# Performance work log

Hardware: AMD Instinct MI355X
Metric: run time of the kernel (lower is better)

Reference implementation:

```python
import jax, jax.numpy as jnp
import numpy as np

B, N, H, KRATE = 128, 400, 128, 0.2
EPS = 1e-9


def setup_inputs() -> dict:
    key = jax.random.key(0)
    ks = jax.random.split(key, 16)
    # correlation-like input: symmetric, values in (-1,1), unit diagonal
    x = jax.random.normal(ks[0], (B, N, N), dtype=jnp.float32)
    x = jnp.tanh(0.3 * x)
    x = 0.5 * (x + x.transpose(0, 2, 1))
    eye = jnp.eye(N, dtype=jnp.float32)
    x = x * (1.0 - eye) + eye

    def lin(k, fan_in, shape):
        return jax.random.normal(k, shape, dtype=jnp.float32) / np.sqrt(fan_in).astype(np.float32)

    return {
        "x": x,
        "slength": jnp.full((B,), 100, dtype=jnp.int32),
        # AE denoiser (num_of_node=N, hidden=H)
        "enc1_w": lin(ks[1], N, (N, H)), "enc1_b": jnp.zeros((H,), jnp.float32),
        "enc2_w": lin(ks[2], N, (N, H)), "enc2_b": jnp.zeros((H,), jnp.float32),
        "dec2_w": lin(ks[3], H, (H, N)), "dec2_b": jnp.zeros((N,), jnp.float32),
        "dec1_w": lin(ks[4], H, (H, N)), "dec1_b": jnp.zeros((N,), jnp.float32),
        # GCN predictor
        "gcn1_w": lin(ks[5], N, (N, H)), "gcn1_b": jnp.zeros((H,), jnp.float32),
        "gcn2_w": lin(ks[6], H, (H, H)), "gcn2_b": jnp.zeros((H,), jnp.float32),
        # classification head Linear(128 -> 2)
        "fc_w": lin(ks[7], H, (H, 2)), "fc_b": jnp.zeros((2,), jnp.float32),
    }


def reference(x, slength, enc1_w, enc1_b, enc2_w, enc2_b, dec2_w, dec2_b,
              dec1_w, dec1_b, gcn1_w, gcn1_b, gcn2_w, gcn2_b, fc_w, fc_b):
    eye = jnp.eye(N, dtype=x.dtype)

    # fisher transform + normalize by [0,0] entry
    xf = 0.5 * jnp.log((1.0 + x + EPS) / (1.0 - x + EPS))
    xf = xf / xf[:, 0, 0][:, None, None]

    # --- DA / AE denoiser: deltax = AE(xf), symmetrized ---
    out1 = jax.nn.relu(jnp.einsum('bij,jh->bih', xf, enc1_w) + enc1_b).transpose(0, 2, 1)  # [B,H,N]
    out2 = jax.nn.relu(jnp.einsum('bhn,nk->bhk', out1, enc2_w) + enc2_b)                   # [B,H,H]
    out2 = jax.nn.relu(jnp.einsum('bhk,kn->bhn', out2, dec2_w) + dec2_b + out1)            # [B,H,N]
    out2 = out2.transpose(0, 2, 1)                                                         # [B,N,H]
    delta = jnp.einsum('bnh,hm->bnm', out2, dec1_w) + dec1_b                               # [B,N,N]
    delta = 0.5 * (delta + delta.transpose(0, 2, 1))
    x2 = xf + delta * (1.0 - eye)

    # --- predictor on detached x2 ---
    xp = jax.lax.stop_gradient(x2)

    # topk sparsification at rate 0.2 over flattened NxN per sample
    k = int(N * N * KRATE)
    flat = xp.reshape(B, N * N)
    _, idx = jax.lax.top_k(flat, k)
    mask = jnp.zeros((B, N * N), xp.dtype).at[jnp.arange(B)[:, None], idx].set(1.0)
    A = xp * mask.reshape(B, N, N)

    # GCN norm (PyG gcn_norm with add_remaining_self_loops, fill=1)
    diag = jnp.diagonal(A, axis1=1, axis2=2)
    A = A + eye[None] * jnp.where(diag == 0.0, 1.0, 0.0)[:, :, None]
    deg = A.sum(axis=1)                      # scatter of edge weight on col index
    dinv = deg ** -0.5
    dinv = jnp.where(jnp.isinf(dinv), 0.0, dinv)
    An = dinv[:, :, None] * A * dinv[:, None, :]  # An[b,i,j] = dinv[i]*A[i,j]*dinv[j]

    # GCNConv1 -> ReLU -> GCNConv2 (aggregate onto col/target index)
    h = jax.nn.relu(jnp.einsum('bij,bif->bjf', An, xp @ gcn1_w) + gcn1_b)  # [B,N,H]
    h = jnp.einsum('bij,bif->bjf', An, h @ gcn2_w) + gcn2_b                # [B,N,H]

    pooled = h.mean(axis=1)                  # mean over nodes -> [B,H]
    out = jax.nn.relu(pooled) @ fc_w + fc_b  # [B,2]
    return out
```

## Files before the change

### kernel.cpp

```cpp
#include <hip/hip_runtime.h>
#include <hip/hip_bf16.h>
#include <math.h>

#define BATCH 128
#define NNODE 400
#define HID   128
#define NN    (NNODE*NNODE)
#define KSEL  32000
#define EQCAP 1024
#define EPSF  1e-9f
#define TSPLIT 8
#define SEG   (NN / TSPLIT)
#define NT    7
#define KC400 14
#define FRAGS (KC400*4096)
#define PLA   57344

__device__ __forceinline__ unsigned tokey(float f) {
  unsigned u = __float_as_uint(f);
  return (u & 0x80000000u) ? ~u : (u | 0x80000000u);
}

__device__ __forceinline__ short f2bf(float f) {
  unsigned u = __float_as_uint(f);
  u += 0x7fffu + ((u >> 16) & 1u);
  return (short)(u >> 16);
}
__device__ __forceinline__ float bf2f(short s) {
  return __uint_as_float(((unsigned)(unsigned short)s) << 16);
}

typedef __attribute__((ext_vector_type(8))) short s8v;
typedef __attribute__((ext_vector_type(4))) short s4v;
typedef __attribute__((ext_vector_type(4))) float f4v;

#define BK 16
#define LP 68

template<bool AT, bool BIAS, bool RES, bool RELU, bool TS>
__global__ void __launch_bounds__(256) gemm64(
    const float* __restrict__ A, long sA, int lda,
    const float* __restrict__ B, long sB, int ldb,
    const float* __restrict__ bias,
    const float* __restrict__ Res, long sRes,
    float* __restrict__ C, long sC, int ldc,
    int M, int Nc, int K)
{
  __shared__ float As[BK][LP];
  __shared__ float Bs[BK][LP];
  const int bz = blockIdx.z;
  A += (size_t)bz * sA;
  B += (size_t)bz * sB;
  C += (size_t)bz * sC;
  const float* Rp = RES ? (Res + (size_t)bz * sRes) : nullptr;

  const int n0 = blockIdx.x * 64;
  const int m0 = blockIdx.y * 64;
  const int tid = threadIdx.x;
  const int tx = tid & 15, ty = tid >> 4;
  const bool edgeM = (m0 + 64 > M);
  const bool edgeN = (n0 + 64 > Nc);

  float acc[4][4];
#pragma unroll
  for (int i = 0; i < 4; ++i)
#pragma unroll
    for (int j = 0; j < 4; ++j) acc[i][j] = 0.f;

  for (int k0 = 0; k0 < K; k0 += BK) {
    if (!AT) {
      const int m = tid & 63, g = tid >> 6;
      if (!edgeM) {
        const float4 v = *(const float4*)(A + (size_t)(m0 + m) * lda + k0 + 4 * g);
        As[4 * g + 0][m] = v.x; As[4 * g + 1][m] = v.y;
        As[4 * g + 2][m] = v.z; As[4 * g + 3][m] = v.w;
      } else {
        const int gm = m0 + m;
        const bool ok = gm < M;
#pragma unroll
        for (int j = 0; j < 4; ++j)
          As[4 * g + j][m] = ok ? A[(size_t)gm * lda + k0 + 4 * g + j] : 0.f;
      }
    } else {
      const int k = tid >> 4, mg = tid & 15;
      if (!edgeM) {
        const float4 v = *(const float4*)(A + (size_t)(k0 + k) * lda + m0 + 4 * mg);
        *(float4*)&As[k][4 * mg] = v;
      } else {
#pragma unroll
        for (int j = 0; j < 4; ++j) {
          const int gm = m0 + 4 * mg + j;
          As[k][4 * mg + j] = (gm < M) ? A[(size_t)(k0 + k) * lda + gm] : 0.f;
        }
      }
    }
    {
      const int k = tid >> 4, ng = tid & 15;
      if (!edgeN) {
        const float4 v = *(const float4*)(B + (size_t)(k0 + k) * ldb + n0 + 4 * ng);
        *(float4*)&Bs[k][4 * ng] = v;
      } else {
#pragma unroll
        for (int j = 0; j < 4; ++j) {
          const int gn = n0 + 4 * ng + j;
          Bs[k][4 * ng + j] = (gn < Nc) ? B[(size_t)(k0 + k) * ldb + gn] : 0.f;
        }
      }
    }
    __syncthreads();
#pragma unroll
    for (int kk = 0; kk < BK; ++kk) {
      const float4 a = *(const float4*)&As[kk][ty << 2];
      const float4 b = *(const float4*)&Bs[kk][tx << 2];
      const float av[4] = {a.x, a.y, a.z, a.w};
      const float bv[4] = {b.x, b.y, b.z, b.w};
#pragma unroll
      for (int i = 0; i < 4; ++i)
#pragma unroll
        for (int j = 0; j < 4; ++j) acc[i][j] += av[i] * bv[j];
    }
    __syncthreads();
  }

#pragma unroll
  for (int i = 0; i < 4; ++i) {
    const int m = m0 + (ty << 2) + i;
    if (m >= M) continue;
#pragma unroll
    for (int j = 0; j < 4; ++j) {
      const int n = n0 + (tx << 2) + j;
      if (n >= Nc) continue;
      float v = acc[i][j];
      if (BIAS) v += bias[n];
      const size_t loc = TS ? ((size_t)n * ldc + m) : ((size_t)m * ldc + n);
      if (RES) v += Rp[loc];
      if (RELU) v = fmaxf(v, 0.f);
      C[loc] = v;
    }
  }
}

__global__ void bsplitN(const float* __restrict__ W, int K, int Kpad,
                        int N, int Npad, short* __restrict__ out) {
  int t = blockIdx.x * 256 + threadIdx.x;
  if (t >= Kpad * Npad) return;
  int k = t / Npad, n = t - k * Npad;
  float v = (k < K && n < N) ? W[(size_t)k * N + n] : 0.f;
  short hi = f2bf(v);
  short lo = f2bf(v - bf2f(hi));
  int ntiles = Npad >> 4;
  size_t idx = (((size_t)(k >> 5) * ntiles + (n >> 4)) * 64
                + (((k >> 3) & 3) * 16 + (n & 15))) * 8 + (k & 7);
  size_t PL = (size_t)(Kpad >> 5) * ntiles * 512;
  out[idx] = hi;
  out[PL + idx] = lo;
}

__global__ void afrag(const float* __restrict__ src, short* __restrict__ dst) {
  int t = blockIdx.x * 256 + threadIdx.x;
  if (t >= BATCH * 4 * 4 * 28 * 16) return;
  int l = t & 15; t >>= 4;
  int mt = t % 28; t /= 28;
  int quad = t & 3; t >>= 2;
  int c = t & 3; t >>= 2;
  int b = t;
  int m = mt * 16 + l;
  int kb = c * 32 + quad * 8;
  const float* p = src + (size_t)b * HID * NNODE + (size_t)kb * NNODE + m;
  s8v hi, lo;
#pragma unroll
  for (int j = 0; j < 8; ++j) {
    float v = (m < NNODE) ? p[(size_t)j * NNODE] : 0.f;
    short h = f2bf(v);
    hi[j] = h; lo[j] = f2bf(v - bf2f(h));
  }
  size_t o = (size_t)b * 2 * PLA + (((size_t)c * 28 + mt) * 64 + quad * 16 + l) * 8;
  *(s8v*)(dst + o) = hi;
  *(s8v*)(dst + o + PLA) = lo;
}

template<bool AT, bool FRAG, bool BIAS, bool RELU, bool SCL, bool TS>
__global__ void __launch_bounds__(256) mfgemm(
    const float* __restrict__ A, long sA, int lda,
    const short* __restrict__ Bf, long sB, int kc,
    const float* __restrict__ bias,
    const float* __restrict__ scl,
    float* __restrict__ Cf, long sCf, int ldc,
    short* __restrict__ Cfrag, long sCfrag, int okc,
    int M, int K)
{
  __shared__ float As[64][68];
  const int bz = blockIdx.y;
  A += (size_t)bz * sA;
  Bf += (size_t)bz * sB;
  if (SCL) scl += (size_t)bz * NNODE;
  if (!FRAG) Cf += (size_t)bz * sCf;
  else       Cfrag += (size_t)bz * sCfrag;

  const int tid = threadIdx.x;
  const int lane = tid & 63, wave = tid >> 6;
  const int wqm = wave >> 1, wqn = wave & 1;
  const int quad = lane >> 4, l15 = lane & 15;
  const int m0 = blockIdx.x * 64;

  f4v acc[2][4];
#pragma unroll
  for (int i = 0; i < 2; ++i)
#pragma unroll
    for (int j = 0; j < 4; ++j) acc[i][j] = (f4v){0.f, 0.f, 0.f, 0.f};

  const int nstage = (K + 63) >> 6;
  for (int st = 0; st < nstage; ++st) {
    const int k0 = st << 6;
    if (st) __syncthreads();
    if (!AT) {
      const int mrow = tid >> 4;
      const int k4 = (tid & 15) << 2;
#pragma unroll
      for (int u = 0; u < 4; ++u) {
        const int m = mrow + (u << 4);
        const int gm = m0 + m, gk = k0 + k4;
        float4 v = {0.f, 0.f, 0.f, 0.f};
        if (gm < M) {
          if (gk + 4 <= K) v = *(const float4*)(A + (size_t)gm * lda + gk);
          else {
            float* pv = (float*)&v;
#pragma unroll
            for (int j = 0; j < 4; ++j)
              if (gk + j < K) pv[j] = A[(size_t)gm * lda + gk + j];
          }
        }
        *(float4*)&As[m][k4] = v;
      }
    } else {
      const int kk = tid >> 4;
      const int m4 = (tid & 15) << 2;
#pragma unroll
      for (int u = 0; u < 4; ++u) {
        const int gk = k0 + kk + (u << 4);
        float4 v = {0.f, 0.f, 0.f, 0.f};
        if (gk < K) {
          if (m0 + m4 + 4 <= M) v = *(const float4*)(A + (size_t)gk * lda + m0 + m4);
          else {
            float* pv = (float*)&v;
#pragma unroll
            for (int j = 0; j < 4; ++j)
              if (m0 + m4 + j < M) pv[j] = A[(size_t)gk * lda + m0 + m4 + j];
          }
        }
        As[m4 + 0][kk + (u << 4)] = v.x;
        As[m4 + 1][kk + (u << 4)] = v.y;
        As[m4 + 2][kk + (u << 4)] = v.z;
        As[m4 + 3][kk + (u << 4)] = v.w;
      }
    }
    __syncthreads();

#pragma unroll
    for (int c2 = 0; c2 < 2; ++c2) {
      const int c = (st << 1) + c2;
      s8v bhi[4], blo[4];
#pragma unroll
      for (int nt = 0; nt < 4; ++nt) {
        const int ntg = (wqn << 2) + nt;
        const size_t off = (((size_t)c * 8 + ntg) * 64 + lane) * 8;
        bhi[nt] = *(const s8v*)(Bf + off);
        blo[nt] = *(const s8v*)(Bf + (size_t)kc * 4096 + off);
      }
#pragma unroll
      for (int mt = 0; mt < 2; ++mt) {
        const int row = (wqm << 5) + (mt << 4) + l15;
        const int kof = (c2 << 5) + (quad << 3);
        const f4v a0 = *(const f4v*)&As[row][kof];
        const f4v a1 = *(const f4v*)&As[row][kof + 4];
        s8v ah, al;
#pragma unroll
        for (int j = 0; j < 4; ++j) {
          short h0 = f2bf(a0[j]); ah[j] = h0; al[j] = f2bf(a0[j] - bf2f(h0));
          short h1 = f2bf(a1[j]); ah[j + 4] = h1; al[j + 4] = f2bf(a1[j] - bf2f(h1));
        }
#pragma unroll
        for (int nt = 0; nt < 4; ++nt) {
          acc[mt][nt] = __builtin_amdgcn_mfma_f32_16x16x32_bf16(ah, bhi[nt], acc[mt][nt], 0, 0, 0);
          acc[mt][nt] = __builtin_amdgcn_mfma_f32_16x16x32_bf16(ah, blo[nt], acc[mt][nt], 0, 0, 0);
          acc[mt][nt] = __builtin_amdgcn_mfma_f32_16x16x32_bf16(al, bhi[nt], acc[mt][nt], 0, 0, 0);
        }
      }
    }
  }

  if (TS) {
    for (int nh = 0; nh < 2; ++nh) {
      __syncthreads();
      if (wqn == nh) {
#pragma unroll
        for (int mt = 0; mt < 2; ++mt)
#pragma unroll
          for (int nt = 0; nt < 4; ++nt) {
            const int tn = (nt << 4) + l15;
            const int n  = (wqn << 6) + tn;
            const int mc = (wqm << 5) + (mt << 4) + (quad << 2);
            const f4v a = acc[mt][nt];
#pragma unroll
            for (int reg = 0; reg < 4; ++reg) {
              float v = a[reg];
              if (SCL) v *= scl[m0 + mc + reg];
              if (BIAS) v += bias[n];
              if (RELU) v = fmaxf(v, 0.f);
              As[tn][mc + reg] = v;
            }
          }
      }
      __syncthreads();
      const int row = tid >> 2, cq = tid & 3;
#pragma unroll
      for (int u = 0; u < 4; ++u) {
        const int col = (cq + (u << 2)) << 2;
        if (m0 + col + 4 <= M) {
          const float4 v = *(const float4*)&As[row][col];
          *(float4*)(Cf + (size_t)((nh << 6) + row) * ldc + m0 + col) = v;
        }
      }
    }
    return;
  }

#pragma unroll
  for (int mt = 0; mt < 2; ++mt) {
    const int mb = m0 + (wqm << 5) + (mt << 4) + (quad << 2);
#pragma unroll
    for (int nt = 0; nt < 4; ++nt) {
      const int n = (wqn << 6) + (nt << 4) + l15;
      const f4v a = acc[mt][nt];
      if (!FRAG) {
#pragma unroll
        for (int reg = 0; reg < 4; ++reg) {
          const int m = mb + reg;
          if (m < M) {
            float v = a[reg];
            if (SCL) v *= scl[m];
            if (BIAS) v += bias[n];
            if (RELU) v = fmaxf(v, 0.f);
            Cf[(size_t)m * ldc + n] = v;
          }
        }
      } else {
        s4v h4, l4;
#pragma unroll
        for (int reg = 0; reg < 4; ++reg) {
          const int m = mb + reg;
          float v = (m < M) ? (SCL ? a[reg] * scl[m] : a[reg]) : 0.f;
          short hh = f2bf(v);
          h4[reg] = hh; l4[reg] = f2bf(v - bf2f(hh));
        }
        const int chunkT = mb >> 5, quadT = (mb >> 3) & 3, jT0 = mb & 7;
        const size_t off = (((size_t)chunkT * 8 + (wqn << 2) + nt) * 64
                            + quadT * 16 + l15) * 8 + jT0;
        *(s4v*)(Cfrag + off) = h4;
        *(s4v*)(Cfrag + (size_t)okc * 4096 + off) = l4;
      }
    }
  }
}

__global__ void __launch_bounds__(256) g4mf(
    const short* __restrict__ o1f,
    const short* __restrict__ wfrag,
    const float* __restrict__ bias,
    float* __restrict__ xf,
    unsigned* __restrict__ ghist)
{
  __shared__ float D2[64][68];
  __shared__ unsigned hist[8][256];
  const int b = blockIdx.y;
  int p = blockIdx.x, bi = 0;
  while (p >= NT - bi) { p -= NT - bi; ++bi; }
  const int bj = bi + p;
  const int I0 = bi * 64, J0 = bj * 64;
  const bool diag = (bi == bj);

  o1f += (size_t)b * 2 * PLA;
  xf += (size_t)b * NN;
  unsigned* gh = ghist + b * 256;

  const int tid = threadIdx.x;
  const int lane = tid & 63, wave = tid >> 6;
  const int wq = wave & 1;
  const bool d1 = wave < 2;
  const int At = (d1 ? bi : bj) * 4;
  const int Bt = (d1 ? bj : bi) * 4;
  const int quad = lane >> 4, l15 = lane & 15;

  for (int i = tid; i < 8 * 256; i += 256) ((unsigned*)hist)[i] = 0u;

  f4v acc[2][4];
#pragma unroll
  for (int i = 0; i < 2; ++i)
#pragma unroll
    for (int j = 0; j < 4; ++j) acc[i][j] = (f4v){0.f, 0.f, 0.f, 0.f};

  for (int c = 0; c < 4; ++c) {
    s8v ahi[2], alo[2];
#pragma unroll
    for (int mt = 0; mt < 2; ++mt) {
      const int mtg = At + (wq << 1) + mt;
      const size_t off = (((size_t)c * 28 + mtg) * 64 + lane) * 8;
      ahi[mt] = *(const s8v*)(o1f + off);
      alo[mt] = *(const s8v*)(o1f + PLA + off);
    }
    s8v bhi[4], blo[4];
#pragma unroll
    for (int nt = 0; nt < 4; ++nt) {
      const int ntg = Bt + nt;
      const size_t off = (((size_t)c * 28 + ntg) * 64 + lane) * 8;
      bhi[nt] = *(const s8v*)(wfrag + off);
      blo[nt] = *(const s8v*)(wfrag + PLA + off);
    }
#pragma unroll
    for (int mt = 0; mt < 2; ++mt)
#pragma unroll
      for (int nt = 0; nt < 4; ++nt) {
        acc[mt][nt] = __builtin_amdgcn_mfma_f32_16x16x32_bf16(ahi[mt], bhi[nt], acc[mt][nt], 0, 0, 0);
        acc[mt][nt] = __builtin_amdgcn_mfma_f32_16x16x32_bf16(ahi[mt], blo[nt], acc[mt][nt], 0, 0, 0);
        acc[mt][nt] = __builtin_amdgcn_mfma_f32_16x16x32_bf16(alo[mt], bhi[nt], acc[mt][nt], 0, 0, 0);
      }
  }
  __syncthreads();

  if (!d1) {
#pragma unroll
    for (int mt = 0; mt < 2; ++mt) {
      const int mb = (wq << 5) + (mt << 4) + (quad << 2);
#pragma unroll
      for (int nt = 0; nt < 4; ++nt) {
        const int nn = (nt << 4) + l15;
        const f4v a = acc[mt][nt];
#pragma unroll
        for (int reg = 0; reg < 4; ++reg) D2[mb + reg][nn] = a[reg];
      }
    }
  }
  __syncthreads();

  if (d1) {
    const int rep = tid & 7;
#pragma unroll
    for (int mt = 0; mt < 2; ++mt) {
      const int a0 = (wq << 5) + (mt << 4) + (quad << 2);
#pragma unroll
      for (int nt = 0; nt < 4; ++nt) {
        const int nn = (nt << 4) + l15;
        const int gj = J0 + nn;
        const f4v d1v = acc[mt][nt];
        const f4v d2t = *(const f4v*)&D2[nn][a0];
        f4v vv;
#pragma unroll
        for (int reg = 0; reg < 4; ++reg) {
          const int gi = I0 + a0 + reg;
          float v = 0.f;
          if (gi < NNODE && gj < NNODE) {
            v = xf[(size_t)gi * NNODE + gj];
            if (gi != gj)
              v += 0.5f * (d1v[reg] + d2t[reg] + bias[gj] + bias[gi]);
            atomicAdd(&hist[rep][tokey(v) >> 24], diag ? 1u : 2u);
          }
          vv[reg] = v;
        }
#pragma unroll
        for (int reg = 0; reg < 4; ++reg) {
          const int gi = I0 + a0 + reg;
          if (gi < NNODE && gj < NNODE) xf[(size_t)gi * NNODE + gj] = vv[reg];
        }
        if (!diag && gj < NNODE && (I0 + a0 + 4 <= NNODE)) {
          *(float4*)(xf + (size_t)gj * NNODE + I0 + a0) = *(float4*)&vv;
        }
      }
    }
  }
  __syncthreads();
  if (tid < 256) {
    const unsigned s = hist[0][tid] + hist[1][tid] + hist[2][tid] + hist[3][tid]
                     + hist[4][tid] + hist[5][tid] + hist[6][tid] + hist[7][tid];
    if (s) atomicAdd(&gh[tid], s);
  }
}

__global__ void denom_k(const float* __restrict__ x, float* __restrict__ denom) {
  int b = threadIdx.x;
  if (b < BATCH) {
    float v = x[(size_t)b * NN];
    denom[b] = 0.5f * logf((1.0f + v + EPSF) / (1.0f - v + EPSF));
  }
}

__global__ void xf_k(const float* __restrict__ x, const float* __restrict__ denom,
                     float* __restrict__ xf) {
  size_t e = (size_t)blockIdx.x * 256 + threadIdx.x;
  if (e >= (size_t)BATCH * NN) return;
  int b = (int)(e / NN);
  float v = x[e];
  float t = 0.5f * logf((1.0f + v + EPSF) / (1.0f - v + EPSF));
  xf[e] = t / denom[b];
}

__global__ void tz_init(unsigned* __restrict__ ghist, unsigned* __restrict__ sprefix,
                        int* __restrict__ sk, int* __restrict__ eqcnt) {
  int t = blockIdx.x * 256 + threadIdx.x;
  if (t < BATCH * 256) ghist[t] = 0u;
  if (t < BATCH) { sprefix[t] = 0u; sk[t] = KSEL; eqcnt[t] = 0; }
}

template<int PASS>
__global__ void __launch_bounds__(256) thist(const float* __restrict__ x2,
                                             const unsigned* __restrict__ sprefix,
                                             unsigned* __restrict__ ghist) {
  constexpr int shift = 24 - 8 * PASS;
  __shared__ unsigned h[8][256];
  const int b  = blockIdx.y;
  const int sb = blockIdx.x;
  const int tid = threadIdx.x;
  for (int i = tid; i < 8 * 256; i += 256) ((unsigned*)h)[i] = 0u;
  __syncthreads();

  const unsigned prefix = sprefix[b];
  const unsigned pmask  = 0xFFFFFFFFu << (shift + 8);
  const int rep = tid & 7;
  const float4* p4 = (const float4*)(x2 + (size_t)b * NN);
  const int i0 = sb * (SEG / 4), i1 = i0 + (SEG / 4);
  for (int i = i0 + tid; i < i1; i += 256) {
    float4 v = p4[i];
    unsigned k0 = tokey(v.x), k1 = tokey(v.y), k2 = tokey(v.z), k3 = tokey(v.w);
    if ((k0 & pmask) == prefix) atomicAdd(&h[rep][(k0 >> shift) & 255u], 1u);
    if ((k1 & pmask) == prefix) atomicAdd(&h[rep][(k1 >> shift) & 255u], 1u);
    if ((k2 & pmask) == prefix) atomicAdd(&h[rep][(k2 >> shift) & 255u], 1u);
    if ((k3 & pmask) == prefix) atomicAdd(&h[rep][(k3 >> shift) & 255u], 1u);
  }
  __syncthreads();
  if (tid < 256) {
    unsigned s = h[0][tid] + h[1][tid] + h[2][tid] + h[3][tid]
               + h[4][tid] + h[5][tid] + h[6][tid] + h[7][tid];
    if (s) atomicAdd(&ghist[b * 256 + tid], s);
  }
}

template<int PASS>
__global__ void __launch_bounds__(256) tpick(unsigned* __restrict__ ghist,
                                             unsigned* __restrict__ sprefix,
                                             int* __restrict__ sk,
                                             unsigned* __restrict__ tau,
                                             int* __restrict__ rrem) {
  constexpr int shift = 24 - 8 * PASS;
  const int b = blockIdx.x;
  __shared__ unsigned h[256];
  h[threadIdx.x] = ghist[b * 256 + threadIdx.x];
  __syncthreads();
  if (threadIdx.x == 0) {
    int k = sk[b];
    unsigned byte = 0u;
    for (int bin = 255; bin >= 0; --bin) {
      int c = (int)h[bin];
      if (c >= k) { byte = (unsigned)bin; break; }
      k -= c;
    }
    unsigned np = sprefix[b] | (byte << shift);
    sprefix[b] = np; sk[b] = k;
    if (PASS == 3) { tau[b] = np; rrem[b] = k; }
  }
  ghist[b * 256 + threadIdx.x] = 0u;
}

__global__ void build_k(const float* __restrict__ x2, const unsigned* __restrict__ tau,
                        float* __restrict__ A, int* __restrict__ eqcnt,
                        int* __restrict__ eqidx) {
  size_t e = (size_t)blockIdx.x * 256 + threadIdx.x;
  if (e >= (size_t)BATCH * NN) return;
  int b = (int)(e / NN);
  int i = (int)(e - (size_t)b * NN);
  float v = x2[e];
  unsigned key = tokey(v);
  unsigned tk = tau[b];
  A[e] = (key > tk) ? v : 0.f;
  if (key == tk) {
    int p = atomicAdd(&eqcnt[b], 1);
    if (p < EQCAP) eqidx[b * EQCAP + p] = i;
  }
}

__global__ void eqfix_k(float* __restrict__ A, const float* __restrict__ x2,
                        const int* __restrict__ eqcnt, const int* __restrict__ eqidx,
                        const int* __restrict__ rrem) {
  int b = blockIdx.x;
  int cnt = eqcnt[b]; if (cnt > EQCAP) cnt = EQCAP;
  int r = rrem[b];
  for (int t = threadIdx.x; t < cnt; t += 256) {
    int idx = eqidx[b * EQCAP + t];
    int rank = 0;
    for (int u = 0; u < cnt; ++u) rank += (eqidx[b * EQCAP + u] < idx) ? 1 : 0;
    if (rank < r) A[(size_t)b * NN + idx] = x2[(size_t)b * NN + idx];
  }
}

__global__ void diag_k(float* __restrict__ A) {
  int t = blockIdx.x * blockDim.x + threadIdx.x;
  if (t >= BATCH * NNODE) return;
  int b = t / NNODE, i = t - b * NNODE;
  size_t o = (size_t)b * NN + (size_t)i * NNODE + i;
  if (A[o] == 0.f) A[o] = 1.0f;
}

__global__ void deg_k(const float* __restrict__ A, float* __restrict__ dinv) {
  int t = blockIdx.x * blockDim.x + threadIdx.x;
  if (t >= BATCH * NNODE) return;
  int b = t / NNODE, j = t - b * NNODE;
  const float* p = A + (size_t)b * NN + j;
  float s = 0.f;
  for (int i = 0; i < NNODE; ++i) s += p[(size_t)i * NNODE];
  dinv[t] = (s == 0.f) ? 0.f : 1.0f / sqrtf(s);
}

__global__ void head_k(const float* __restrict__ h2, const float* __restrict__ fc_w,
                       const float* __restrict__ fc_b, float* __restrict__ out) {
  int b = blockIdx.x;
  int f = threadIdx.x;
  float s = 0.f;
  const float* p = h2 + (size_t)b * NNODE * HID + f;
  for (int j = 0; j < NNODE; ++j) s += p[(size_t)j * HID];
  float pv = fmaxf(s / (float)NNODE, 0.f);
  __shared__ float r0[128], r1[128];
  r0[f] = pv * fc_w[f * 2 + 0];
  r1[f] = pv * fc_w[f * 2 + 1];
  __syncthreads();
  for (int sft = 64; sft > 0; sft >>= 1) {
    if (f < sft) { r0[f] += r0[f + sft]; r1[f] += r1[f + sft]; }
    __syncthreads();
  }
  if (f == 0) {
    out[b * 2 + 0] = r0[0] + fc_b[0];
    out[b * 2 + 1] = r1[0] + fc_b[1];
  }
}

extern "C" void kernel_launch(void* const* d_in, const int* in_sizes, int n_in,
                              void* d_out, int out_size, void* d_ws, size_t ws_size,
                              hipStream_t stream) {
  const float* x      = (const float*)d_in[0];
  const float* enc1_w = (const float*)d_in[2];
  const float* enc1_b = (const float*)d_in[3];
  const float* enc2_w = (const float*)d_in[4];
  const float* enc2_b = (const float*)d_in[5];
  const float* dec2_w = (const float*)d_in[6];
  const float* dec2_b = (const float*)d_in[7];
  const float* dec1_w = (const float*)d_in[8];
  const float* dec1_b = (const float*)d_in[9];
  const float* gcn1_w = (const float*)d_in[10];
  const float* gcn1_b = (const float*)d_in[11];
  const float* gcn2_w = (const float*)d_in[12];
  const float* gcn2_b = (const float*)d_in[13];
  const float* fc_w   = (const float*)d_in[14];
  const float* fc_b   = (const float*)d_in[15];
  float* out = (float*)d_out;
  (void)in_sizes; (void)n_in; (void)out_size; (void)ws_size;

  float* ws = (float*)d_ws;
  size_t off = 0;
  auto take = [&](size_t n) { float* p = ws + off; off += (n + 63) & ~(size_t)63; return p; };
  float* xf   = take((size_t)BATCH * NN);
  float* dl   = take((size_t)BATCH * NN);
  float* o1   = take((size_t)BATCH * HID * NNODE);
  float* o2   = take((size_t)BATCH * HID * HID);
  float* hbuf = take((size_t)BATCH * NNODE * HID);
  float* denom = take(BATCH);
  float* dinv  = take((size_t)BATCH * NNODE);
  unsigned* tau = (unsigned*)take(BATCH);
  int* rrem  = (int*)take(BATCH);
  int* eqcnt = (int*)take(BATCH);
  int* eqidx = (int*)take((size_t)BATCH * EQCAP);
  unsigned* ghist   = (unsigned*)take((size_t)BATCH * 256);
  unsigned* sprefix = (unsigned*)take(BATCH);
  int*      sk      = (int*)take(BATCH);
  short* w1frag = (short*)take((size_t)FRAGS + 64);
  short* w2frag = (short*)take((size_t)4 * 4096 + 64);
  short* e1frag = (short*)take((size_t)FRAGS + 64);
  short* e2frag = (short*)take((size_t)FRAGS + 64);
  short* dfrag  = (short*)take((size_t)PLA + 64);
  short* xwfrag = (short*)o1;
  short* o1f    = (short*)dl;
  const long sXW = 2L * FRAGS;

  const size_t TOT = (size_t)BATCH * NN;
  const int EW_BLK = (int)((TOT + 255) / 256);

  tz_init<<<128, 256, 0, stream>>>(ghist, sprefix, sk, eqcnt);
  denom_k<<<1, BATCH, 0, stream>>>(x, denom);
  xf_k<<<EW_BLK, 256, 0, stream>>>(x, denom, xf);
  bsplitN<<<224, 256, 0, stream>>>(gcn1_w, NNODE, 448, HID, 128, w1frag);
  bsplitN<<<64,  256, 0, stream>>>(gcn2_w, HID, 128, HID, 128, w2frag);
  bsplitN<<<224, 256, 0, stream>>>(enc1_w, NNODE, 448, HID, 128, e1frag);
  bsplitN<<<224, 256, 0, stream>>>(enc2_w, NNODE, 448, HID, 128, e2frag);
  bsplitN<<<224, 256, 0, stream>>>(dec1_w, HID, 128, NNODE, 448, dfrag);

  mfgemm<false, false, true, true, false, true><<<dim3(7, BATCH), 256, 0, stream>>>(
      xf, NN, NNODE, e1frag, 0, KC400, enc1_b, nullptr,
      o1, (long)HID * NNODE, NNODE, nullptr, 0, 0, NNODE, NNODE);
  mfgemm<false, false, true, true, false, false><<<dim3(2, BATCH), 256, 0, stream>>>(
      o1, (long)HID * NNODE, NNODE, e2frag, 0, KC400, enc2_b, nullptr,
      o2, (long)HID * HID, HID, nullptr, 0, 0, HID, NNODE);
  gemm64<false, true, true, true, false><<<dim3(7, 2, BATCH), 256, 0, stream>>>(
      o2, (long)HID * HID, HID, dec2_w, 0, NNODE, dec2_b,
      o1, (long)HID * NNODE, o1, (long)HID * NNODE, NNODE, HID, NNODE, HID);

  afrag<<<3584, 256, 0, stream>>>(o1, o1f);
  g4mf<<<dim3(NT * (NT + 1) / 2, BATCH), 256, 0, stream>>>(o1f, dfrag, dec1_b, xf, ghist);

  tpick<0><<<BATCH, 256, 0, stream>>>(ghist, sprefix, sk, tau, rrem);
  thist<1><<<dim3(TSPLIT, BATCH), 256, 0, stream>>>(xf, sprefix, ghist);
  tpick<1><<<BATCH, 256, 0, stream>>>(ghist, sprefix, sk, tau, rrem);
  thist<2><<<dim3(TSPLIT, BATCH), 256, 0, stream>>>(xf, sprefix, ghist);
  tpick<2><<<BATCH, 256, 0, stream>>>(ghist, sprefix, sk, tau, rrem);
  thist<3><<<dim3(TSPLIT, BATCH), 256, 0, stream>>>(xf, sprefix, ghist);
  tpick<3><<<BATCH, 256, 0, stream>>>(ghist, sprefix, sk, tau, rrem);

  build_k<<<EW_BLK, 256, 0, stream>>>(xf, tau, dl, eqcnt, eqidx);
  eqfix_k<<<BATCH, 256, 0, stream>>>(dl, xf, eqcnt, eqidx, rrem);
  diag_k<<<(BATCH * NNODE + 255) / 256, 256, 0, stream>>>(dl);
  deg_k<<<(BATCH * NNODE + 255) / 256, 256, 0, stream>>>(dl, dinv);

  mfgemm<false, true, false, false, true, false><<<dim3(7, BATCH), 256, 0, stream>>>(
      xf, NN, NNODE, w1frag, 0, KC400, nullptr, dinv,
      nullptr, 0, 128, xwfrag, sXW, KC400, NNODE, NNODE);
  mfgemm<true, false, true, true, true, false><<<dim3(7, BATCH), 256, 0, stream>>>(
      dl, NN, NNODE, xwfrag, sXW, KC400, gcn1_b, dinv,
      hbuf, (long)NNODE * HID, HID, nullptr, 0, 0, NNODE, NNODE);
  mfgemm<false, true, false, false, true, false><<<dim3(7, BATCH), 256, 0, stream>>>(
      hbuf, (long)NNODE * HID, HID, w2frag, 0, 4, nullptr, dinv,
      nullptr, 0, 128, xwfrag, sXW, KC400, NNODE, HID);
  mfgemm<true, false, true, false, true, false><<<dim3(7, BATCH), 256, 0, stream>>>(
      dl, NN, NNODE, xwfrag, sXW, KC400, gcn2_b, dinv,
      hbuf, (long)NNODE * HID, HID, nullptr, 0, 0, NNODE, NNODE);

  head_k<<<BATCH, HID, 0, stream>>>(hbuf, fc_w, fc_b, out);
}
```

Measured before the change: 701.9 us.

## Fuse Fisher transform, fragment packing and degree sums into neighbouring kernels

```diff
diff --git a/kernel.cpp b/kernel.cpp
--- a/kernel.cpp
+++ b/kernel.cpp
@@ -156,30 +156,7 @@
   out[PL + idx] = lo;
 }
 
-__global__ void afrag(const float* __restrict__ src, short* __restrict__ dst) {
-  int t = blockIdx.x * 256 + threadIdx.x;
-  if (t >= BATCH * 4 * 4 * 28 * 16) return;
-  int l = t & 15; t >>= 4;
-  int mt = t % 28; t /= 28;
-  int quad = t & 3; t >>= 2;
-  int c = t & 3; t >>= 2;
-  int b = t;
-  int m = mt * 16 + l;
-  int kb = c * 32 + quad * 8;
-  const float* p = src + (size_t)b * HID * NNODE + (size_t)kb * NNODE + m;
-  s8v hi, lo;
-#pragma unroll
-  for (int j = 0; j < 8; ++j) {
-    float v = (m < NNODE) ? p[(size_t)j * NNODE] : 0.f;
-    short h = f2bf(v);
-    hi[j] = h; lo[j] = f2bf(v - bf2f(h));
-  }
-  size_t o = (size_t)b * 2 * PLA + (((size_t)c * 28 + mt) * 64 + quad * 16 + l) * 8;
-  *(s8v*)(dst + o) = hi;
-  *(s8v*)(dst + o + PLA) = lo;
-}
-
-template<bool AT, bool FRAG, bool BIAS, bool RELU, bool SCL, bool TS>
+template<bool AT, bool FRAG, bool BIAS, bool RELU, bool SCL, bool TS, bool XF>
 __global__ void __launch_bounds__(256) mfgemm(
     const float* __restrict__ A, long sA, int lda,
     const short* __restrict__ Bf, long sB, int kc,
@@ -187,6 +164,7 @@
     const float* __restrict__ scl,
     float* __restrict__ Cf, long sCf, int ldc,
     short* __restrict__ Cfrag, long sCfrag, int okc,
+    const float* __restrict__ denomp, float* __restrict__ xfout,
     int M, int K)
 {
   __shared__ float As[64][68];
@@ -196,6 +174,8 @@
   if (SCL) scl += (size_t)bz * NNODE;
   if (!FRAG) Cf += (size_t)bz * sCf;
   else       Cfrag += (size_t)bz * sCfrag;
+  if (XF) xfout += (size_t)bz * sA;
+  const float dnm = XF ? denomp[bz] : 0.f;
 
   const int tid = threadIdx.x;
   const int lane = tid & 63, wave = tid >> 6;
@@ -222,12 +202,26 @@
         const int gm = m0 + m, gk = k0 + k4;
         float4 v = {0.f, 0.f, 0.f, 0.f};
         if (gm < M) {
-          if (gk + 4 <= K) v = *(const float4*)(A + (size_t)gm * lda + gk);
-          else {
+          if (gk + 4 <= K) {
+            float4 xv = *(const float4*)(A + (size_t)gm * lda + gk);
+            if (XF) {
+              v.x = 0.5f * logf((1.0f + xv.x + EPSF) / (1.0f - xv.x + EPSF)) / dnm;
+              v.y = 0.5f * logf((1.0f + xv.y + EPSF) / (1.0f - xv.y + EPSF)) / dnm;
+              v.z = 0.5f * logf((1.0f + xv.z + EPSF) / (1.0f - xv.z + EPSF)) / dnm;
+              v.w = 0.5f * logf((1.0f + xv.w + EPSF) / (1.0f - xv.w + EPSF)) / dnm;
+              *(float4*)(xfout + (size_t)gm * lda + gk) = v;
+            } else v = xv;
+          } else {
             float* pv = (float*)&v;
 #pragma unroll
             for (int j = 0; j < 4; ++j)
-              if (gk + j < K) pv[j] = A[(size_t)gm * lda + gk + j];
+              if (gk + j < K) {
+                float xv = A[(size_t)gm * lda + gk + j];
+                if (XF) {
+                  pv[j] = 0.5f * logf((1.0f + xv + EPSF) / (1.0f - xv + EPSF)) / dnm;
+                  xfout[(size_t)gm * lda + gk + j] = pv[j];
+                } else pv[j] = xv;
+              }
           }
         }
         *(float4*)&As[m][k4] = v;
@@ -364,13 +358,13 @@
 }
 
 __global__ void __launch_bounds__(256) g4mf(
-    const short* __restrict__ o1f,
+    const float* __restrict__ o1,
     const short* __restrict__ wfrag,
     const float* __restrict__ bias,
     float* __restrict__ xf,
     unsigned* __restrict__ ghist)
 {
-  __shared__ float D2[64][68];
+  __shared__ float S[2 * 64 * 36];
   __shared__ unsigned hist[8][256];
   const int b = blockIdx.y;
   int p = blockIdx.x, bi = 0;
@@ -379,7 +373,7 @@
   const int I0 = bi * 64, J0 = bj * 64;
   const bool diag = (bi == bj);
 
-  o1f += (size_t)b * 2 * PLA;
+  o1 += (size_t)b * HID * NNODE;
   xf += (size_t)b * NN;
   unsigned* gh = ghist + b * 256;
 
@@ -387,10 +381,13 @@
   const int lane = tid & 63, wave = tid >> 6;
   const int wq = wave & 1;
   const bool d1 = wave < 2;
-  const int At = (d1 ? bi : bj) * 4;
   const int Bt = (d1 ? bj : bi) * 4;
   const int quad = lane >> 4, l15 = lane & 15;
 
+  float* SI = S;
+  float* SJ = S + 64 * 36;
+  const float* Sp = d1 ? SI : SJ;
+
   for (int i = tid; i < 8 * 256; i += 256) ((unsigned*)hist)[i] = 0u;
 
   f4v acc[2][4];
@@ -400,14 +397,37 @@
     for (int j = 0; j < 4; ++j) acc[i][j] = (f4v){0.f, 0.f, 0.f, 0.f};
 
   for (int c = 0; c < 4; ++c) {
-    s8v ahi[2], alo[2];
-#pragma unroll
-    for (int mt = 0; mt < 2; ++mt) {
-      const int mtg = At + (wq << 1) + mt;
-      const size_t off = (((size_t)c * 28 + mtg) * 64 + lane) * 8;
-      ahi[mt] = *(const s8v*)(o1f + off);
-      alo[mt] = *(const s8v*)(o1f + PLA + off);
-    }
+    const int k0 = c << 5;
+    if (c) __syncthreads();
+    {
+      const int kk = tid >> 4;
+      const int m4 = (tid & 15) << 2;
+#pragma unroll
+      for (int half = 0; half < 2; ++half) {
+        const int k = k0 + kk + (half << 4);
+        const float* row = o1 + (size_t)k * NNODE;
+        float4 vi = {0.f,0.f,0.f,0.f}, vj = {0.f,0.f,0.f,0.f};
+        if (I0 + m4 + 4 <= NNODE) vi = *(const float4*)(row + I0 + m4);
+        else {
+          float* pv = (float*)&vi;
+#pragma unroll
+          for (int j = 0; j < 4; ++j) if (I0 + m4 + j < NNODE) pv[j] = row[I0 + m4 + j];
+        }
+        if (J0 + m4 + 4 <= NNODE) vj = *(const float4*)(row + J0 + m4);
+        else {
+          float* pv = (float*)&vj;
+#pragma unroll
+          for (int j = 0; j < 4; ++j) if (J0 + m4 + j < NNODE) pv[j] = row[J0 + m4 + j];
+        }
+        const int kc2 = kk + (half << 4);
+        SI[(m4 + 0) * 36 + kc2] = vi.x; SI[(m4 + 1) * 36 + kc2] = vi.y;
+        SI[(m4 + 2) * 36 + kc2] = vi.z; SI[(m4 + 3) * 36 + kc2] = vi.w;
+        SJ[(m4 + 0) * 36 + kc2] = vj.x; SJ[(m4 + 1) * 36 + kc2] = vj.y;
+        SJ[(m4 + 2) * 36 + kc2] = vj.z; SJ[(m4 + 3) * 36 + kc2] = vj.w;
+      }
+    }
+    __syncthreads();
+
     s8v bhi[4], blo[4];
 #pragma unroll
     for (int nt = 0; nt < 4; ++nt) {
@@ -417,16 +437,27 @@
       blo[nt] = *(const s8v*)(wfrag + PLA + off);
     }
 #pragma unroll
-    for (int mt = 0; mt < 2; ++mt)
+    for (int mt = 0; mt < 2; ++mt) {
+      const int m = ((wq << 1) + mt) * 16 + l15;
+      const f4v a0 = *(const f4v*)&Sp[m * 36 + (quad << 3)];
+      const f4v a1 = *(const f4v*)&Sp[m * 36 + (quad << 3) + 4];
+      s8v ah, al;
+#pragma unroll
+      for (int j = 0; j < 4; ++j) {
+        short h0 = f2bf(a0[j]); ah[j] = h0; al[j] = f2bf(a0[j] - bf2f(h0));
+        short h1 = f2bf(a1[j]); ah[j + 4] = h1; al[j + 4] = f2bf(a1[j] - bf2f(h1));
+      }
 #pragma unroll
       for (int nt = 0; nt < 4; ++nt) {
-        acc[mt][nt] = __builtin_amdgcn_mfma_f32_16x16x32_bf16(ahi[mt], bhi[nt], acc[mt][nt], 0, 0, 0);
-        acc[mt][nt] = __builtin_amdgcn_mfma_f32_16x16x32_bf16(ahi[mt], blo[nt], acc[mt][nt], 0, 0, 0);
-        acc[mt][nt] = __builtin_amdgcn_mfma_f32_16x16x32_bf16(alo[mt], bhi[nt], acc[mt][nt], 0, 0, 0);
-      }
-  }
-  __syncthreads();
-
+        acc[mt][nt] = __builtin_amdgcn_mfma_f32_16x16x32_bf16(ah, bhi[nt], acc[mt][nt], 0, 0, 0);
+        acc[mt][nt] = __builtin_amdgcn_mfma_f32_16x16x32_bf16(ah, blo[nt], acc[mt][nt], 0, 0, 0);
+        acc[mt][nt] = __builtin_amdgcn_mfma_f32_16x16x32_bf16(al, bhi[nt], acc[mt][nt], 0, 0, 0);
+      }
+    }
+  }
+  __syncthreads();
+
+  float (*D2)[68] = (float(*)[68])S;
   if (!d1) {
 #pragma unroll
     for (int mt = 0; mt < 2; ++mt) {
@@ -493,21 +524,13 @@
   }
 }
 
-__global__ void xf_k(const float* __restrict__ x, const float* __restrict__ denom,
-                     float* __restrict__ xf) {
-  size_t e = (size_t)blockIdx.x * 256 + threadIdx.x;
-  if (e >= (size_t)BATCH * NN) return;
-  int b = (int)(e / NN);
-  float v = x[e];
-  float t = 0.5f * logf((1.0f + v + EPSF) / (1.0f - v + EPSF));
-  xf[e] = t / denom[b];
-}
-
 __global__ void tz_init(unsigned* __restrict__ ghist, unsigned* __restrict__ sprefix,
-                        int* __restrict__ sk, int* __restrict__ eqcnt) {
+                        int* __restrict__ sk, int* __restrict__ eqcnt,
+                        float* __restrict__ deg) {
   int t = blockIdx.x * 256 + threadIdx.x;
   if (t < BATCH * 256) ghist[t] = 0u;
   if (t < BATCH) { sprefix[t] = 0u; sk[t] = KSEL; eqcnt[t] = 0; }
+  if (t < BATCH * NNODE) deg[t] = 0.f;
 }
 
 template<int PASS>
@@ -569,24 +592,36 @@
   ghist[b * 256 + threadIdx.x] = 0u;
 }
 
-__global__ void build_k(const float* __restrict__ x2, const unsigned* __restrict__ tau,
-                        float* __restrict__ A, int* __restrict__ eqcnt,
-                        int* __restrict__ eqidx) {
-  size_t e = (size_t)blockIdx.x * 256 + threadIdx.x;
-  if (e >= (size_t)BATCH * NN) return;
-  int b = (int)(e / NN);
-  int i = (int)(e - (size_t)b * NN);
-  float v = x2[e];
-  unsigned key = tokey(v);
-  unsigned tk = tau[b];
-  A[e] = (key > tk) ? v : 0.f;
-  if (key == tk) {
-    int p = atomicAdd(&eqcnt[b], 1);
-    if (p < EQCAP) eqidx[b * EQCAP + p] = i;
-  }
+__global__ void __launch_bounds__(256) build_kc(
+    const float* __restrict__ x2, const unsigned* __restrict__ tau,
+    float* __restrict__ A, float* __restrict__ deg,
+    int* __restrict__ eqcnt, int* __restrict__ eqidx) {
+  __shared__ float cs[NNODE];
+  const int b = blockIdx.y, rg = blockIdx.x;
+  const int tid = threadIdx.x;
+  for (int i = tid; i < NNODE; i += 256) cs[i] = 0.f;
+  __syncthreads();
+  const unsigned tk = tau[b];
+  const size_t base = (size_t)b * NN + (size_t)rg * 6400;
+  for (int u = 0; u < 25; ++u) {
+    const int t = u * 256 + tid;
+    const float v = x2[base + t];
+    const unsigned key = tokey(v);
+    const float a = (key > tk) ? v : 0.f;
+    A[base + t] = a;
+    if (key == tk) {
+      int p = atomicAdd(&eqcnt[b], 1);
+      if (p < EQCAP) eqidx[b * EQCAP + p] = rg * 6400 + t;
+    }
+    if (a != 0.f) atomicAdd(&cs[t % NNODE], a);
+  }
+  __syncthreads();
+  for (int j = tid; j < NNODE; j += 256)
+    if (cs[j] != 0.f) atomicAdd(&deg[b * NNODE + j], cs[j]);
 }
 
 __global__ void eqfix_k(float* __restrict__ A, const float* __restrict__ x2,
+                        float* __restrict__ deg,
                         const int* __restrict__ eqcnt, const int* __restrict__ eqidx,
                         const int* __restrict__ rrem) {
   int b = blockIdx.x;
@@ -596,26 +631,23 @@
     int idx = eqidx[b * EQCAP + t];
     int rank = 0;
     for (int u = 0; u < cnt; ++u) rank += (eqidx[b * EQCAP + u] < idx) ? 1 : 0;
-    if (rank < r) A[(size_t)b * NN + idx] = x2[(size_t)b * NN + idx];
-  }
-}
-
-__global__ void diag_k(float* __restrict__ A) {
-  int t = blockIdx.x * blockDim.x + threadIdx.x;
-  if (t >= BATCH * NNODE) return;
-  int b = t / NNODE, i = t - b * NNODE;
-  size_t o = (size_t)b * NN + (size_t)i * NNODE + i;
-  if (A[o] == 0.f) A[o] = 1.0f;
-}
-
-__global__ void deg_k(const float* __restrict__ A, float* __restrict__ dinv) {
+    if (rank < r) {
+      float v = x2[(size_t)b * NN + idx];
+      A[(size_t)b * NN + idx] = v;
+      atomicAdd(&deg[b * NNODE + idx % NNODE], v);
+    }
+  }
+}
+
+__global__ void dinv_k(float* __restrict__ A, const float* __restrict__ deg,
+                       float* __restrict__ dinv) {
   int t = blockIdx.x * blockDim.x + threadIdx.x;
   if (t >= BATCH * NNODE) return;
   int b = t / NNODE, j = t - b * NNODE;
-  const float* p = A + (size_t)b * NN + j;
-  float s = 0.f;
-  for (int i = 0; i < NNODE; ++i) s += p[(size_t)i * NNODE];
-  dinv[t] = (s == 0.f) ? 0.f : 1.0f / sqrtf(s);
+  float d = deg[t];
+  size_t o = (size_t)b * NN + (size_t)j * NNODE + j;
+  if (A[o] == 0.f) { A[o] = 1.0f; d += 1.0f; }
+  dinv[t] = (d == 0.f) ? 0.f : 1.0f / sqrtf(d);
 }
 
 __global__ void head_k(const float* __restrict__ h2, const float* __restrict__ fc_w,
@@ -671,6 +703,7 @@
   float* hbuf = take((size_t)BATCH * NNODE * HID);
   float* denom = take(BATCH);
   float* dinv  = take((size_t)BATCH * NNODE);
+  float* deg   = take((size_t)BATCH * NNODE);
   unsigned* tau = (unsigned*)take(BATCH);
   int* rrem  = (int*)take(BATCH);
   int* eqcnt = (int*)take(BATCH);
@@ -684,33 +717,27 @@
   short* e2frag = (short*)take((size_t)FRAGS + 64);
   short* dfrag  = (short*)take((size_t)PLA + 64);
   short* xwfrag = (short*)o1;
-  short* o1f    = (short*)dl;
   const long sXW = 2L * FRAGS;
 
-  const size_t TOT = (size_t)BATCH * NN;
-  const int EW_BLK = (int)((TOT + 255) / 256);
-
-  tz_init<<<128, 256, 0, stream>>>(ghist, sprefix, sk, eqcnt);
+  tz_init<<<200, 256, 0, stream>>>(ghist, sprefix, sk, eqcnt, deg);
   denom_k<<<1, BATCH, 0, stream>>>(x, denom);
-  xf_k<<<EW_BLK, 256, 0, stream>>>(x, denom, xf);
   bsplitN<<<224, 256, 0, stream>>>(gcn1_w, NNODE, 448, HID, 128, w1frag);
   bsplitN<<<64,  256, 0, stream>>>(gcn2_w, HID, 128, HID, 128, w2frag);
   bsplitN<<<224, 256, 0, stream>>>(enc1_w, NNODE, 448, HID, 128, e1frag);
   bsplitN<<<224, 256, 0, stream>>>(enc2_w, NNODE, 448, HID, 128, e2frag);
   bsplitN<<<224, 256, 0, stream>>>(dec1_w, HID, 128, NNODE, 448, dfrag);
 
-  mfgemm<false, false, true, true, false, true><<<dim3(7, BATCH), 256, 0, stream>>>(
-      xf, NN, NNODE, e1frag, 0, KC400, enc1_b, nullptr,
-      o1, (long)HID * NNODE, NNODE, nullptr, 0, 0, NNODE, NNODE);
-  mfgemm<false, false, true, true, false, false><<<dim3(2, BATCH), 256, 0, stream>>>(
+  mfgemm<false, false, true, true, false, true, true><<<dim3(7, BATCH), 256, 0, stream>>>(
+      x, NN, NNODE, e1frag, 0, KC400, enc1_b, nullptr,
+      o1, (long)HID * NNODE, NNODE, nullptr, 0, 0, denom, xf, NNODE, NNODE);
+  mfgemm<false, false, true, true, false, false, false><<<dim3(2, BATCH), 256, 0, stream>>>(
       o1, (long)HID * NNODE, NNODE, e2frag, 0, KC400, enc2_b, nullptr,
-      o2, (long)HID * HID, HID, nullptr, 0, 0, HID, NNODE);
+      o2, (long)HID * HID, HID, nullptr, 0, 0, nullptr, nullptr, HID, NNODE);
   gemm64<false, true, true, true, false><<<dim3(7, 2, BATCH), 256, 0, stream>>>(
       o2, (long)HID * HID, HID, dec2_w, 0, NNODE, dec2_b,
       o1, (long)HID * NNODE, o1, (long)HID * NNODE, NNODE, HID, NNODE, HID);
 
-  afrag<<<3584, 256, 0, stream>>>(o1, o1f);
-  g4mf<<<dim3(NT * (NT + 1) / 2, BATCH), 256, 0, stream>>>(o1f, dfrag, dec1_b, xf, ghist);
+  g4mf<<<dim3(NT * (NT + 1) / 2, BATCH), 256, 0, stream>>>(o1, dfrag, dec1_b, xf, ghist);
 
   tpick<0><<<BATCH, 256, 0, stream>>>(ghist, sprefix, sk, tau, rrem);
   thist<1><<<dim3(TSPLIT, BATCH), 256, 0, stream>>>(xf, sprefix, ghist);
@@ -720,23 +747,22 @@
   thist<3><<<dim3(TSPLIT, BATCH), 256, 0, stream>>>(xf, sprefix, ghist);
   tpick<3><<<BATCH, 256, 0, stream>>>(ghist, sprefix, sk, tau, rrem);
 
-  build_k<<<EW_BLK, 256, 0, stream>>>(xf, tau, dl, eqcnt, eqidx);
-  eqfix_k<<<BATCH, 256, 0, stream>>>(dl, xf, eqcnt, eqidx, rrem);
-  diag_k<<<(BATCH * NNODE + 255) / 256, 256, 0, stream>>>(dl);
-  deg_k<<<(BATCH * NNODE + 255) / 256, 256, 0, stream>>>(dl, dinv);
-
-  mfgemm<false, true, false, false, true, false><<<dim3(7, BATCH), 256, 0, stream>>>(
+  build_kc<<<dim3(25, BATCH), 256, 0, stream>>>(xf, tau, dl, deg, eqcnt, eqidx);
+  eqfix_k<<<BATCH, 256, 0, stream>>>(dl, xf, deg, eqcnt, eqidx, rrem);
+  dinv_k<<<(BATCH * NNODE + 255) / 256, 256, 0, stream>>>(dl, deg, dinv);
+
+  mfgemm<false, true, false, false, true, false, false><<<dim3(7, BATCH), 256, 0, stream>>>(
       xf, NN, NNODE, w1frag, 0, KC400, nullptr, dinv,
-      nullptr, 0, 128, xwfrag, sXW, KC400, NNODE, NNODE);
-  mfgemm<true, false, true, true, true, false><<<dim3(7, BATCH), 256, 0, stream>>>(
+      nullptr, 0, 128, xwfrag, sXW, KC400, nullptr, nullptr, NNODE, NNODE);
+  mfgemm<true, false, true, true, true, false, false><<<dim3(7, BATCH), 256, 0, stream>>>(
       dl, NN, NNODE, xwfrag, sXW, KC400, gcn1_b, dinv,
-      hbuf, (long)NNODE * HID, HID, nullptr, 0, 0, NNODE, NNODE);
-  mfgemm<false, true, false, false, true, false><<<dim3(7, BATCH), 256, 0, stream>>>(
+      hbuf, (long)NNODE * HID, HID, nullptr, 0, 0, nullptr, nullptr, NNODE, NNODE);
+  mfgemm<false, true, false, false, true, false, false><<<dim3(7, BATCH), 256, 0, stream>>>(
       hbuf, (long)NNODE * HID, HID, w2frag, 0, 4, nullptr, dinv,
-      nullptr, 0, 128, xwfrag, sXW, KC400, NNODE, HID);
-  mfgemm<true, false, true, false, true, false><<<dim3(7, BATCH), 256, 0, stream>>>(
+      nullptr, 0, 128, xwfrag, sXW, KC400, nullptr, nullptr, NNODE, HID);
+  mfgemm<true, false, true, false, true, false, false><<<dim3(7, BATCH), 256, 0, stream>>>(
       dl, NN, NNODE, xwfrag, sXW, KC400, gcn2_b, dinv,
-      hbuf, (long)NNODE * HID, HID, nullptr, 0, 0, NNODE, NNODE);
+      hbuf, (long)NNODE * HID, HID, nullptr, 0, 0, nullptr, nullptr, NNODE, NNODE);
 
   head_k<<<BATCH, HID, 0, stream>>>(hbuf, fc_w, fc_b, out);
 }
```

After: 690.6 us. About the same (-1.6%).
